# Optimization experiments

Measured on AMD Instinct MI355X. Metric: run time of the kernel, lower is better.

Reference implementation:

```python
import jax, jax.numpy as jnp
import numpy as np

B, S, L, CIN = 8, 32, 128, 1024
C1, C2 = 512, 256            # conv1_channel, conv2_channel
D1, D2 = 512, 128            # deconv1_channel, deconv2_channel
CD, SIM = 300, 128           # concept_dim, similarity_dim
L4 = L // 4


def _conv1d(x, w, b, pad):
    # x: [N, Cin, L], w: [Cout, Cin, k] (PyTorch layout)
    y = jax.lax.conv_general_dilated(x, w, (1,), [(pad, pad)],
                                     dimension_numbers=('NCH', 'OIH', 'NCH'))
    return y + b[None, :, None]


def _maxpool2(x):
    return jax.lax.reduce_window(x, -jnp.inf, jax.lax.max, (1, 1, 2), (1, 1, 2), 'VALID')


def _deconv1d(x, w, b):
    # PyTorch ConvTranspose1d(kernel=4, stride=2, padding=1); w: [Cin, Cout, k]
    w2 = jnp.flip(w, -1).transpose(1, 0, 2)  # -> OIH
    y = jax.lax.conv_general_dilated(x, w2, (1,), [(2, 2)], lhs_dilation=(2,),
                                     dimension_numbers=('NCH', 'OIH', 'NCH'))
    return y + b[None, :, None]


def setup_inputs():
    ks = jax.random.split(jax.random.key(0), 32)
    g = lambda i, shape: jax.random.normal(ks[i], shape, jnp.float32) * 0.02
    return {
        'batch': jax.random.normal(ks[0], (B, S, L, CIN), jnp.float32),
        'concept1': jax.random.normal(ks[1], (B, CD), jnp.float32),
        'concept2': jax.random.normal(ks[2], (B, CD), jnp.float32),
        'seg_len': jax.random.randint(ks[3], (B, S), 1, L + 1),
        'conv1_w': g(4, (C1, CIN, 5)), 'conv1_b': g(5, (C1,)),
        'conv2_w': g(6, (C2, C1, 5)), 'conv2_b': g(7, (C2,)),
        'sa_wq': g(8, (C2, C2)), 'sa_bq': g(9, (C2,)),
        'sa_wk': g(10, (C2, C2)), 'sa_bk': g(11, (C2,)),
        'sa_v': g(12, (C2,)), 'sa_vb': g(13, ()),
        'ca_wq': g(14, (CD, C2)), 'ca_bq': g(15, (C2,)),
        'ca_wk': g(16, (C2, C2)), 'ca_bk': g(17, (C2,)),
        'ca_v': g(18, (C2,)), 'ca_vb': g(19, ()),
        'dc1_w': g(20, (4 * C2, D1, 4)), 'dc1_b': g(21, (D1,)),
        'dc2_w': g(22, (D1, D2, 4)), 'dc2_b': g(23, (D2,)),
        'sim1_w': g(24, (D2, SIM)),
        'sim2_w': g(25, (CD, SIM)),
        'mlp_w': g(26, (SIM,)), 'mlp_b': g(27, ()),
    }


def reference(batch, concept1, concept2, seg_len,
              conv1_w, conv1_b, conv2_w, conv2_b,
              sa_wq, sa_bq, sa_wk, sa_bk, sa_v, sa_vb,
              ca_wq, ca_bq, ca_wk, ca_bk, ca_v, ca_vb,
              dc1_w, dc1_b, dc2_w, dc2_b,
              sim1_w, sim2_w, mlp_w, mlp_b):
    N = B * S
    # conv stack: [N, CIN, L] -> [N, C2, L/4]
    x = batch.reshape(N, L, CIN).transpose(0, 2, 1)
    t = _maxpool2(_conv1d(x, conv1_w, conv1_b, 2))
    t = _maxpool2(_conv1d(t, conv2_w, conv2_b, 2))
    tmp2 = t.transpose(0, 2, 1)                       # [N, L4, C2]

    # vectorized length mask: mask[i,j,k] = k < ceil(seg_len/4)  <=>  seg_len > 4k
    mask = (seg_len[:, :, None] > 4 * jnp.arange(L4)).reshape(N, 1, L4)

    # self additive attention over pooled positions
    qp = tmp2 @ sa_wq + sa_bq                          # [N, L4, H]
    kp = tmp2 @ sa_wk + sa_bk                          # [N, L4, H]
    s = jnp.einsum('nqkh,h->nqk', jnp.tanh(qp[:, :, None, :] + kp[:, None, :, :]), sa_v) + sa_vb
    s = jnp.where(mask, s, -1e9)
    a = jax.nn.softmax(s, axis=-1)                     # [N, L4, L4]
    self_res = jnp.einsum('nqk,nkc->nqc', a, tmp2)     # [N, L4, C2]

    # concept attention (query identical across positions -> compute once)
    ckp = tmp2 @ ca_wk + ca_bk                         # [N, L4, H]

    def concept_attn(c):
        cq = jnp.repeat(c @ ca_wq + ca_bq, S, axis=0)  # [N, H]
        sc = jnp.einsum('nkh,h->nk', jnp.tanh(cq[:, None, :] + ckp), ca_v) + ca_vb
        sc = jnp.where(mask[:, 0, :], sc, -1e9)
        ac = jax.nn.softmax(sc, axis=-1)               # [N, L4]
        r = jnp.einsum('nk,nkc->nc', ac, tmp2)         # [N, C2]
        return jnp.broadcast_to(r[:, None, :], (N, L4, C2))

    c1_res = concept_attn(concept1)
    c2_res = concept_attn(concept2)

    ar = jnp.concatenate([tmp2, self_res, c1_res, c2_res], axis=-1)  # [N, L4, 4*C2]
    r = _deconv1d(ar.transpose(0, 2, 1), dc1_w, dc1_b)               # [N, D1, L/2]
    r = _deconv1d(r, dc2_w, dc2_b).transpose(0, 2, 1)                # [N, L, D2]
    r = r.reshape(B, S * L, D2)

    sim1 = r @ sim1_w                                                # [B, S*L, SIM]

    def score(c):
        cs = (c @ sim2_w)[:, None, :] * sim1
        return jax.nn.sigmoid(cs @ mlp_w + mlp_b).reshape(B, S, L)

    return score(concept1), score(concept2)
```

## Files before the change

### kernel.cpp

```cpp
#include <hip/hip_runtime.h>
#include <cstdint>

typedef __bf16 bf16;
typedef __bf16 bf16x8 __attribute__((ext_vector_type(8)));
typedef float f32x4 __attribute__((ext_vector_type(4)));

__device__ __forceinline__ void gload_lds16(const void* g, void* l) {
  __builtin_amdgcn_global_load_lds(
      (const __attribute__((address_space(1))) unsigned int*)g,
      (__attribute__((address_space(3))) unsigned int*)l, 16, 0, 0);
}

__device__ __forceinline__ float tanh_fast(float x) {
  float ax = fabsf(x);
  float e = __expf(ax + ax);
  float t = 1.0f - 2.0f / (e + 1.0f);
  return x < 0.0f ? -t : t;
}

template<int MODE, int DEPTH>
__global__ __launch_bounds__(256) void gemm_tap(
    const bf16* __restrict__ A, const bf16* __restrict__ Bt,
    const float* __restrict__ bias, bf16* __restrict__ Out,
    const bf16* __restrict__ zp,
    int snA, int logP, int logCI, int shift0, int ntaps, int cbCount,
    int cbCI, int pairs, int Ktot, int COt, int snO,
    const float* __restrict__ uu, const float* __restrict__ mlpb,
    float* __restrict__ outF)
{
  __shared__ __align__(16) bf16 Ab[2 * DEPTH][4096];
  __shared__ __align__(16) bf16 Bb[2 * DEPTH][4096];
  const int tid  = threadIdx.x;
  const int wave = tid >> 6, lane = tid & 63;
  const int wr = wave >> 1, wc = wave & 1;
  const int m0  = blockIdx.x << 7;
  const int co0 = blockIdx.y << 7;
  const int P     = 1 << logP;
  const int Pmask = P - 1;
  const int CI    = 1 << logCI;
  f32x4 acc[4][4] = {};

  const int rowL = tid >> 2;
  const int kg   = tid & 3;
  const int fOff = ((kg ^ ((rowL + (rowL >> 2)) & 3)) << 3);

  const int mA0 = m0 + rowL,      nA0 = mA0 >> logP, pA0v = mA0 & Pmask;
  const int mA1 = m0 + rowL + 64, nA1 = mA1 >> logP, pA1v = mA1 & Pmask;
  const bf16* baseA0 = A + nA0 * snA + fOff;
  const bf16* baseA1 = A + nA1 * snA + fOff;
  const bf16* baseB0 = Bt + (co0 + rowL) * Ktot + fOff;
  const bf16* baseB1 = Bt + (co0 + rowL + 64) * Ktot + fOff;
  const bf16* zsrc = zp + fOff;

  const int frow  = lane & 15;
  const int rdOff = (((lane >> 4) ^ ((frow + (frow >> 2)) & 3)) << 3);

  for (int cb = 0; cb < cbCount; ++cb) {
    for (int tap = 0; tap < ntaps; ++tap) {
      const int sh = tap + shift0;
      const int rA0 = pA0v + sh, rA1 = pA1v + sh;
      const bool v0 = (unsigned)rA0 < (unsigned)P;
      const bool v1 = (unsigned)rA1 < (unsigned)P;
      const bf16* pa0 = v0 ? (baseA0 + rA0 * CI + cb * cbCI) : zsrc;
      const bf16* pa1 = v1 ? (baseA1 + rA1 * CI + cb * cbCI) : zsrc;
      const bf16* pb0 = baseB0 + (cb * ntaps + tap) * cbCI;
      const bf16* pb1 = baseB1 + (cb * ntaps + tap) * cbCI;

      for (int kc = 0; kc < pairs; kc += DEPTH) {
#pragma unroll
        for (int h = 0; h < 2 * DEPTH; ++h) {
          gload_lds16(pa0 + 32 * h, &Ab[h][wave * 512]);
          gload_lds16(pa1 + 32 * h, &Ab[h][2048 + wave * 512]);
          gload_lds16(pb0 + 32 * h, &Bb[h][wave * 512]);
          gload_lds16(pb1 + 32 * h, &Bb[h][2048 + wave * 512]);
        }
        if (v0) pa0 += 64 * DEPTH;
        if (v1) pa1 += 64 * DEPTH;
        pb0 += 64 * DEPTH; pb1 += 64 * DEPTH;
        __syncthreads();
#pragma unroll
        for (int h = 0; h < 2 * DEPTH; ++h) {
          bf16x8 af[4], bg[4];
#pragma unroll
          for (int i = 0; i < 4; ++i) {
            af[i] = *(const bf16x8*)&Ab[h][((wr << 6) + (i << 4) + frow) * 32 + rdOff];
            bg[i] = *(const bf16x8*)&Bb[h][((wc << 6) + (i << 4) + frow) * 32 + rdOff];
          }
#pragma unroll
          for (int i = 0; i < 4; ++i)
#pragma unroll
            for (int j = 0; j < 4; ++j)
              acc[i][j] = __builtin_amdgcn_mfma_f32_16x16x32_bf16(af[i], bg[j], acc[i][j], 0, 0, 0);
        }
        __syncthreads();
      }
    }
  }

  const int colL = lane & 15;
  const int rq   = (lane >> 4) << 2;

  if (MODE == 2) {
    float* scr0 = (float*)&Ab[0][0];
    float* scr1 = (float*)&Bb[0][0];
    const int n = m0 >> logP;
    const int b = n >> 5;
    const float* u0 = uu + b * 128;
    const float* u1 = uu + 1024 + b * 128;
#pragma unroll
    for (int i = 0; i < 4; ++i) {
#pragma unroll
      for (int r = 0; r < 4; ++r) {
        int rowLcl = (wr << 6) + (i << 4) + rq + r;
        float p0 = 0.0f, p1 = 0.0f;
#pragma unroll
        for (int j = 0; j < 4; ++j) {
          int gco = (wc << 6) + (j << 4) + colL;
          float v = acc[i][j][r];
          p0 += v * u0[gco];
          p1 += v * u1[gco];
        }
        scr0[rowLcl * 32 + (wc << 4) + colL] = p0;
        scr1[rowLcl * 32 + (wc << 4) + colL] = p1;
      }
    }
    __syncthreads();
    {
      int rowLcl = tid >> 1, c = tid & 1;
      const float* s = c ? scr1 : scr0;
      float sum = 0.0f;
#pragma unroll
      for (int k = 0; k < 32; ++k) sum += s[rowLcl * 32 + k];
      float val = 1.0f / (1.0f + __expf(-(sum + mlpb[0])));
      outF[(c ? 32768 : 0) + m0 + rowLcl] = val;
    }
    return;
  }

#pragma unroll
  for (int i = 0; i < 4; ++i) {
    int m = m0 + (wr << 6) + (i << 4) + rq;
    int n = m >> logP, p = m & Pmask;
#pragma unroll
    for (int j = 0; j < 4; ++j) {
      int gco = co0 + (wc << 6) + (j << 4) + colL;
      float bv = bias[gco];
      if (MODE == 1) {
        float v0 = fmaxf(acc[i][j][0], acc[i][j][1]) + bv;
        float v1 = fmaxf(acc[i][j][2], acc[i][j][3]) + bv;
        bf16* o = Out + n * snO + (p >> 1) * COt + gco;
        o[0]   = (bf16)v0;
        o[COt] = (bf16)v1;
      } else {
#pragma unroll
        for (int r = 0; r < 4; ++r)
          Out[n * snO + (p + r) * COt + gco] = (bf16)(acc[i][j][r] + bv);
      }
    }
  }
}

__global__ __launch_bounds__(256) void prep_all(
    const float* __restrict__ conv1_w, const float* __restrict__ conv2_w,
    const float* __restrict__ sa_wq, const float* __restrict__ sa_wk,
    const float* __restrict__ ca_wk, const float* __restrict__ dc1_w,
    const float* __restrict__ dc2_w, const float* __restrict__ sim1_w,
    const float* __restrict__ c1b, const float* __restrict__ c2b,
    const float* __restrict__ sabq, const float* __restrict__ sabk,
    const float* __restrict__ cabk, const float* __restrict__ d1b,
    const float* __restrict__ d2b,
    const float* __restrict__ c1, const float* __restrict__ c2,
    const float* __restrict__ ca_wq, const float* __restrict__ ca_bq,
    const float* __restrict__ sim2_w, const float* __restrict__ mlp_w,
    const float* __restrict__ batch, bf16* __restrict__ bb16,
    bf16* __restrict__ Bt1, bf16* __restrict__ Bt2, bf16* __restrict__ Bqkc,
    bf16* __restrict__ Btd1, bf16* __restrict__ Btd2, bf16* __restrict__ Bts1,
    float* __restrict__ bias, float* __restrict__ cq, float* __restrict__ uu)
{
  const int blk = blockIdx.x;
  if (blk >= 27492) {
    int idx = ((blk - 27492) * 256 + threadIdx.x) * 8;
    float4 a = *(const float4*)&batch[idx];
    float4 b = *(const float4*)&batch[idx + 4];
    bf16x8 v;
    v[0] = (bf16)a.x; v[1] = (bf16)a.y; v[2] = (bf16)a.z; v[3] = (bf16)a.w;
    v[4] = (bf16)b.x; v[5] = (bf16)b.y; v[6] = (bf16)b.z; v[7] = (bf16)b.w;
    *(bf16x8*)&bb16[idx] = v;
    return;
  }
  if (blk < 27468) {
    int idx = blk * 256 + threadIdx.x;
    if (idx < 3072) {
      if (idx < 2944) {
        float v;
        if (idx < 512)       v = c1b[idx];
        else if (idx < 768)  v = c2b[idx - 512];
        else if (idx < 1024) v = sabq[idx - 768];
        else if (idx < 1280) v = sabk[idx - 1024];
        else if (idx < 1536) v = cabk[idx - 1280];
        else if (idx < 2560) v = d1b[(idx - 1536) & 511];
        else if (idx < 2816) v = d2b[(idx - 2560) & 127];
        else                 v = 0.0f;
        bias[idx] = v;
      }
    } else if (idx < 2624512) {
      int i = idx - 3072;
      int co = i / 5120, r = i - co * 5120;
      int cb = r / 1280, r2 = r - cb * 1280;
      int tap = r2 >> 8, cl = r2 & 255;
      Bt1[i] = (bf16)conv1_w[co * 5120 + (cb * 256 + cl) * 5 + tap];
    } else if (idx < 3279872) {
      int i = idx - 2624512;
      int co = i / 2560, r = i - co * 2560;
      int cb = r / 1280, r2 = r - cb * 1280;
      int tap = r2 >> 8, cl = r2 & 255;
      Bt2[i] = (bf16)conv2_w[co * 2560 + (cb * 256 + cl) * 5 + tap];
    } else if (idx < 3476480) {
      int i = idx - 3279872;
      int co = i >> 8, ci = i & 255;
      float v;
      if (co < 256)      v = sa_wq[ci * 256 + co];
      else if (co < 512) v = sa_wk[ci * 256 + (co - 256)];
      else               v = ca_wk[ci * 256 + (co - 512)];
      Bqkc[i] = (bf16)v;
    } else if (idx < 6622208) {
      int i = idx - 3476480;
      int co = i / 3072, r = i - co * 3072;
      int cb = r / 768, r2 = r - cb * 768;
      int tap = r2 >> 8, cl = r2 & 255;
      int ci = cb * 256 + cl;
      int par = co >> 9, c = co & 511;
      int ki = -1;
      if (par == 0) { if (tap == 1) ki = 1; else if (tap == 0) ki = 3; }
      else          { if (tap == 2) ki = 0; else if (tap == 1) ki = 2; }
      Btd1[i] = (ki >= 0) ? (bf16)dc1_w[ci * 2048 + c * 4 + ki] : (bf16)0.0f;
    } else if (idx < 7015424) {
      int i = idx - 6622208;
      int co = i / 1536, r = i - co * 1536;
      int cb = r / 768, r2 = r - cb * 768;
      int tap = r2 >> 8, cl = r2 & 255;
      int ci = cb * 256 + cl;
      int par = co >> 7, c = co & 127;
      int ki = -1;
      if (par == 0) { if (tap == 1) ki = 1; else if (tap == 0) ki = 3; }
      else          { if (tap == 2) ki = 0; else if (tap == 1) ki = 2; }
      Btd2[i] = (ki >= 0) ? (bf16)dc2_w[ci * 512 + c * 4 + ki] : (bf16)0.0f;
    } else {
      int i = idx - 7015424;
      int co = i >> 7, ci = i & 127;
      Bts1[i] = (bf16)sim1_w[ci * 128 + co];
    }
  } else {
    int sub = blk - 27468;
    if (sub < 16) {
      int o = sub * 256 + threadIdx.x;
      int c = o >> 11, b = (o >> 8) & 7, h = o & 255;
      const float* cc = (c ? c2 : c1) + b * 300;
      float acc = ca_bq[h];
      for (int j = 0; j < 300; ++j)
        acc += cc[j] * ca_wq[j * 256 + h];
      cq[o] = acc;
    } else {
      int o = (sub - 16) * 256 + threadIdx.x;
      int c = o >> 10, b = (o >> 7) & 7, m = o & 127;
      const float* cc = (c ? c2 : c1) + b * 300;
      float acc = 0.0f;
      for (int j = 0; j < 300; ++j)
        acc += cc[j] * sim2_w[j * 128 + m];
      uu[o] = acc * mlp_w[m];
    }
  }
}

__global__ __launch_bounds__(256) void kattn(
    const bf16* __restrict__ tmp2, const bf16* __restrict__ qkc,
    const float* __restrict__ sa_v, const float* __restrict__ sa_vb,
    const float* __restrict__ ca_v, const float* __restrict__ ca_vb,
    const float* __restrict__ cq, const int* __restrict__ seg,
    bf16* __restrict__ ar)
{
  const int n = blockIdx.x, tid = threadIdx.x;
  __shared__ __align__(16) bf16 t2[32 * 264];
  __shared__ __align__(16) bf16 bufA[32 * 264];
  __shared__ __align__(16) bf16 bufB[32 * 264];
  __shared__ float sv_s[256], cv_s[256];
  __shared__ float sbc[66];
  __shared__ float sbs[32 * 33];
  const int sl = seg[n];

#pragma unroll
  for (int rr = 0; rr < 4; ++rr) {
    int q = tid + (rr << 8);
    int k = q >> 5, c8 = (q & 31) << 3;
    *(uint4*)&t2[k * 264 + c8]   = *(const uint4*)&tmp2[n * 8192 + k * 256 + c8];
    *(uint4*)&bufA[k * 264 + c8] = *(const uint4*)&qkc[n * 24576 + k * 768 + 512 + c8];
  }
  sv_s[tid] = sa_v[tid];
  cv_s[tid] = ca_v[tid];
  __syncthreads();

  if (tid < 64) {
    int c = tid >> 5, k = tid & 31;
    const float* cqr = cq + (c * 8 + (n >> 5)) * 256;
    float acc = 0.0f;
    for (int h = 0; h < 256; ++h)
      acc += tanh_fast(cqr[h] + (float)bufA[k * 264 + h]) * cv_s[h];
    float sc = acc + ca_vb[0];
    sbc[c * 33 + k] = (sl > (k << 2)) ? sc : -1e9f;
  }
  __syncthreads();

#pragma unroll
  for (int rr = 0; rr < 4; ++rr) {
    int q = tid + (rr << 8);
    int k = q >> 5, c8 = (q & 31) << 3;
    *(uint4*)&bufB[k * 264 + c8] = *(const uint4*)&qkc[n * 24576 + k * 768 + c8];
    *(uint4*)&bufA[k * 264 + c8] = *(const uint4*)&qkc[n * 24576 + k * 768 + 256 + c8];
  }
  if (tid < 2) {
    float* row = &sbc[tid * 33];
    float mx = -1e30f;
    for (int k = 0; k < 32; ++k) mx = fmaxf(mx, row[k]);
    float sum = 0.0f;
    for (int k = 0; k < 32; ++k) { float e = __expf(row[k] - mx); row[k] = e; sum += e; }
    float inv = 1.0f / sum;
    for (int k = 0; k < 32; ++k) row[k] *= inv;
  }
  __syncthreads();

  {
    int col = tid;
    float rr0 = 0.0f, rr1 = 0.0f;
    for (int k = 0; k < 32; ++k) {
      float tv = (float)t2[k * 264 + col];
      rr0 += sbc[k] * tv;
      rr1 += sbc[33 + k] * tv;
    }
    bf16 b0 = (bf16)rr0, b1 = (bf16)rr1;
    bf16* arn = ar + n * 32768;
    for (int q = 0; q < 32; ++q) {
      arn[q * 1024 + col]       = t2[q * 264 + col];
      arn[q * 1024 + 512 + col] = b0;
      arn[q * 1024 + 768 + col] = b1;
    }
  }
  {
    float svb = sa_vb[0];
#pragma unroll
    for (int rr = 0; rr < 4; ++rr) {
      int id = tid + (rr << 8);
      int q = id >> 5, k = id & 31;
      float acc = 0.0f;
      for (int h = 0; h < 256; ++h)
        acc += tanh_fast((float)bufB[q * 264 + h] + (float)bufA[k * 264 + h]) * sv_s[h];
      float sc = acc + svb;
      sbs[q * 33 + k] = (sl > (k << 2)) ? sc : -1e9f;
    }
  }
  __syncthreads();

  if (tid < 32) {
    float* row = &sbs[tid * 33];
    float mx = -1e30f;
    for (int k = 0; k < 32; ++k) mx = fmaxf(mx, row[k]);
    float sum = 0.0f;
    for (int k = 0; k < 32; ++k) { float e = __expf(row[k] - mx); row[k] = e; sum += e; }
    float inv = 1.0f / sum;
    for (int k = 0; k < 32; ++k) row[k] *= inv;
  }
  __syncthreads();

  {
    int col = tid;
    bf16* arn = ar + n * 32768;
    for (int q = 0; q < 32; ++q) {
      float acc = 0.0f;
      for (int k = 0; k < 32; ++k)
        acc += sbs[q * 33 + k] * (float)t2[k * 264 + col];
      arn[q * 1024 + 256 + col] = (bf16)acc;
    }
  }
}

extern "C" void kernel_launch(void* const* d_in, const int* in_sizes, int n_in,
                              void* d_out, int out_size, void* d_ws, size_t ws_size,
                              hipStream_t stream) {
  const float* batch    = (const float*)d_in[0];
  const float* concept1 = (const float*)d_in[1];
  const float* concept2 = (const float*)d_in[2];
  const int*   seg      = (const int*)d_in[3];
  const float* conv1_w  = (const float*)d_in[4];
  const float* conv1_b  = (const float*)d_in[5];
  const float* conv2_w  = (const float*)d_in[6];
  const float* conv2_b  = (const float*)d_in[7];
  const float* sa_wq    = (const float*)d_in[8];
  const float* sa_bq    = (const float*)d_in[9];
  const float* sa_wk    = (const float*)d_in[10];
  const float* sa_bk    = (const float*)d_in[11];
  const float* sa_v     = (const float*)d_in[12];
  const float* sa_vb    = (const float*)d_in[13];
  const float* ca_wq    = (const float*)d_in[14];
  const float* ca_bq    = (const float*)d_in[15];
  const float* ca_wk    = (const float*)d_in[16];
  const float* ca_bk    = (const float*)d_in[17];
  const float* ca_v     = (const float*)d_in[18];
  const float* ca_vb    = (const float*)d_in[19];
  const float* dc1_w    = (const float*)d_in[20];
  const float* dc1_b    = (const float*)d_in[21];
  const float* dc2_w    = (const float*)d_in[22];
  const float* dc2_b    = (const float*)d_in[23];
  const float* sim1_w   = (const float*)d_in[24];
  const float* sim2_w   = (const float*)d_in[25];
  const float* mlp_w    = (const float*)d_in[26];
  const float* mlp_b    = (const float*)d_in[27];

  char* ws = (char*)d_ws;
  bf16* bb16  = (bf16*)(ws + 0);
  bf16* qkcb  = (bf16*)(ws + 0);
  bf16* arb   = (bf16*)(ws + 12582912);
  bf16* d1    = (bf16*)(ws + 29360128);
  bf16* rbuf  = (bf16*)(ws + 46137344);
  bf16* t1    = (bf16*)(ws + 67108864);
  bf16* tmp2b = (bf16*)(ws + 83886080);
  bf16* Bt1   = (bf16*)(ws + 88080384);
  bf16* Bt2   = (bf16*)(ws + 93323264);
  bf16* Bqkc  = (bf16*)(ws + 94633984);
  bf16* Btd1  = (bf16*)(ws + 95027200);
  bf16* Btd2  = (bf16*)(ws + 101318656);
  bf16* Bts1  = (bf16*)(ws + 102105088);
  float* biasall = (float*)(ws + 102137856);
  float* cqb  = (float*)(ws + 102149632);
  float* uub  = (float*)(ws + 102166016);
  const bf16* zp = (const bf16*)(biasall + 2816);
  float* outp = (float*)d_out;

  prep_all<<<43876, 256, 0, stream>>>(
      conv1_w, conv2_w, sa_wq, sa_wk, ca_wk, dc1_w, dc2_w, sim1_w,
      conv1_b, conv2_b, sa_bq, sa_bk, ca_bk, dc1_b, dc2_b,
      concept1, concept2, ca_wq, ca_bq, sim2_w, mlp_w,
      batch, bb16,
      Bt1, Bt2, Bqkc, Btd1, Btd2, Bts1, biasall, cqb, uub);

  gemm_tap<1, 1><<<dim3(256, 4), 256, 0, stream>>>(
      bb16, Bt1, biasall + 0, t1, zp, 131072, 7, 10, -2, 5, 4, 256, 4, 5120, 512, 32768,
      nullptr, nullptr, nullptr);

  gemm_tap<1, 2><<<dim3(128, 2), 256, 0, stream>>>(
      t1, Bt2, biasall + 512, tmp2b, zp, 32768, 6, 9, -2, 5, 2, 256, 4, 2560, 256, 8192,
      nullptr, nullptr, nullptr);

  gemm_tap<0, 2><<<dim3(64, 6), 256, 0, stream>>>(
      tmp2b, Bqkc, biasall + 768, qkcb, zp, 8192, 5, 8, 0, 1, 1, 256, 4, 256, 768, 24576,
      nullptr, nullptr, nullptr);

  kattn<<<256, 256, 0, stream>>>(tmp2b, qkcb, sa_v, sa_vb, ca_v, ca_vb, cqb, seg, arb);

  gemm_tap<0, 2><<<dim3(64, 8), 256, 0, stream>>>(
      arb, Btd1, biasall + 1536, d1, zp, 32768, 5, 10, -1, 3, 4, 256, 4, 3072, 1024, 32768,
      nullptr, nullptr, nullptr);

  gemm_tap<0, 2><<<dim3(128, 2), 256, 0, stream>>>(
      d1, Btd2, biasall + 2560, rbuf, zp, 32768, 6, 9, -1, 3, 2, 256, 4, 1536, 256, 16384,
      nullptr, nullptr, nullptr);

  gemm_tap<2, 2><<<dim3(256, 1), 256, 0, stream>>>(
      rbuf, Bts1, biasall + 2816, nullptr, zp, 16384, 7, 7, 0, 1, 1, 128, 2, 128, 128, 16384,
      uub, mlp_b, outp);
}
```

Baseline: 709.4 us.

## Use 256x256-tile 8-wave pipelined GEMM for conv1 with fused maxpool

```diff
diff --git a/kernel.cpp b/kernel.cpp
--- a/kernel.cpp
+++ b/kernel.cpp
@@ -156,6 +156,118 @@
         for (int r = 0; r < 4; ++r)
           Out[n * snO + (p + r) * COt + gco] = (bf16)(acc[i][j][r] + bv);
       }
+    }
+  }
+}
+
+template<int MH, int KS>
+__device__ __forceinline__ void phase8(
+    const bf16 (&Ab)[2][2][8192], const bf16 (&Bb)[2][2][8192],
+    f32x4 (&acc)[8][4], int buf, int wr, int wc, int frow, int rdOff)
+{
+  bf16x8 af[4], bg[4];
+#pragma unroll
+  for (int ii = 0; ii < 4; ++ii)
+    af[ii] = *(const bf16x8*)&Ab[buf][KS][((wr << 7) + (MH << 6) + (ii << 4) + frow) * 32 + rdOff];
+#pragma unroll
+  for (int j = 0; j < 4; ++j)
+    bg[j] = *(const bf16x8*)&Bb[buf][KS][((wc << 6) + (j << 4) + frow) * 32 + rdOff];
+  __builtin_amdgcn_s_barrier();
+  __builtin_amdgcn_s_setprio(1);
+#pragma unroll
+  for (int ii = 0; ii < 4; ++ii)
+#pragma unroll
+    for (int j = 0; j < 4; ++j)
+      acc[(MH << 2) + ii][j] =
+          __builtin_amdgcn_mfma_f32_16x16x32_bf16(af[ii], bg[j], acc[(MH << 2) + ii][j], 0, 0, 0);
+  __builtin_amdgcn_s_setprio(0);
+}
+
+template<int LOGP, int LOGCI, int SH0, int NTAPS, int CBCNT, int CBCI>
+__global__ __launch_bounds__(512, 2) void gemm8_pool(
+    const bf16* __restrict__ A, const bf16* __restrict__ Bt,
+    const float* __restrict__ bias, bf16* __restrict__ Out,
+    const bf16* __restrict__ zp, int snA, int Ktot, int COt, int snO)
+{
+  __shared__ __align__(16) bf16 Ab[2][2][8192];
+  __shared__ __align__(16) bf16 Bb[2][2][8192];
+  constexpr int P = 1 << LOGP, CI = 1 << LOGCI;
+  constexpr int KPC = CBCI / 64;
+  constexpr int NT = CBCNT * NTAPS * KPC;
+
+  const int tid = threadIdx.x;
+  const int wave = tid >> 6, lane = tid & 63;
+  const int wr = wave >> 2, wc = wave & 3;
+  const int m0 = blockIdx.x << 8, co0 = blockIdx.y << 8;
+  const int n0 = m0 >> LOGP;
+
+  f32x4 acc[8][4] = {};
+
+  const int rowP = tid >> 2;
+  const int kOff = (((tid & 3) ^ ((rowP + (rowP >> 2)) & 3)) << 3);
+  const bf16* baseA = A + n0 * snA + kOff;
+  const bf16* baseB = Bt + (co0 + rowP) * Ktot + kOff;
+  const bf16* zsrc = zp + kOff;
+  const int ldsW = wave << 9;
+
+  const int frow = lane & 15;
+  const int rdOff = (((lane >> 4) ^ ((frow + (frow >> 2)) & 3)) << 3);
+
+  auto stageA = [&](int u, int kh, int bfs) {
+    int cb = u / (NTAPS * KPC);
+    int rem = u - cb * (NTAPS * KPC);
+    int tap = rem / KPC;
+    int kc = rem - tap * KPC;
+    int rA = rowP + tap + SH0;
+    bool v = (unsigned)rA < (unsigned)P;
+    const bf16* p0 = v ? baseA + rA * CI + cb * CBCI + kc * 64 + kh * 32 : zsrc;
+    const bf16* p1 = v ? p0 + snA : zsrc;
+    gload_lds16(p0, &Ab[bfs][kh][ldsW]);
+    gload_lds16(p1, &Ab[bfs][kh][ldsW + 4096]);
+  };
+  auto stageB = [&](int u, int kh, int bfs) {
+    const bf16* p0 = baseB + u * 64 + kh * 32;
+    gload_lds16(p0, &Bb[bfs][kh][ldsW]);
+    gload_lds16(p0 + 128 * Ktot, &Bb[bfs][kh][ldsW + 4096]);
+  };
+
+  stageA(0, 0, 0); stageB(0, 0, 0);
+  stageA(0, 1, 0); stageB(0, 1, 0);
+  stageA(1, 0, 1); stageB(1, 0, 1);
+  asm volatile("s_waitcnt vmcnt(4)" ::: "memory");
+  __builtin_amdgcn_s_barrier();
+
+#pragma unroll 1
+  for (int t = 0; t < NT; ++t) {
+    const int buf = t & 1;
+    if (t + 1 < NT) stageA(t + 1, 1, buf ^ 1);
+    phase8<0, 0>(Ab, Bb, acc, buf, wr, wc, frow, rdOff);
+    __builtin_amdgcn_s_barrier();
+    if (t + 1 < NT) stageB(t + 1, 1, buf ^ 1);
+    phase8<1, 0>(Ab, Bb, acc, buf, wr, wc, frow, rdOff);
+    __builtin_amdgcn_s_barrier();
+    if (t + 2 < NT) stageA(t + 2, 0, buf);
+    phase8<0, 1>(Ab, Bb, acc, buf, wr, wc, frow, rdOff);
+    __builtin_amdgcn_s_barrier();
+    if (t + 2 < NT) stageB(t + 2, 0, buf);
+    phase8<1, 1>(Ab, Bb, acc, buf, wr, wc, frow, rdOff);
+    if (t < NT - 2) { asm volatile("s_waitcnt vmcnt(4)" ::: "memory"); }
+    else            { asm volatile("s_waitcnt vmcnt(0)" ::: "memory"); }
+    __builtin_amdgcn_s_barrier();
+  }
+
+  const int colL = lane & 15, rq = (lane >> 4) << 2;
+#pragma unroll
+  for (int i = 0; i < 8; ++i) {
+    int m = m0 + (wr << 7) + (i << 4) + rq;
+    int n = m >> LOGP, p = m & (P - 1);
+    bf16* orow = Out + n * snO + (p >> 1) * COt;
+#pragma unroll
+    for (int j = 0; j < 4; ++j) {
+      int gco = co0 + (wc << 6) + (j << 4) + colL;
+      float bv = bias[gco];
+      orow[gco]       = (bf16)(fmaxf(acc[i][j][0], acc[i][j][1]) + bv);
+      orow[COt + gco] = (bf16)(fmaxf(acc[i][j][2], acc[i][j][3]) + bv);
     }
   }
 }
@@ -441,9 +553,8 @@
       batch, bb16,
       Bt1, Bt2, Bqkc, Btd1, Btd2, Bts1, biasall, cqb, uub);
 
-  gemm_tap<1, 1><<<dim3(256, 4), 256, 0, stream>>>(
-      bb16, Bt1, biasall + 0, t1, zp, 131072, 7, 10, -2, 5, 4, 256, 4, 5120, 512, 32768,
-      nullptr, nullptr, nullptr);
+  gemm8_pool<7, 10, -2, 5, 4, 256><<<dim3(128, 2), 512, 0, stream>>>(
+      bb16, Bt1, biasall + 0, t1, zp, 131072, 5120, 512, 32768);
 
   gemm_tap<1, 2><<<dim3(128, 2), 256, 0, stream>>>(
       t1, Bt2, biasall + 512, tmp2b, zp, 32768, 6, 9, -2, 5, 2, 256, 4, 2560, 256, 8192,
```

After: 701.0 us. Within noise of the previous version (-1.2%).

## Double-buffer GEMM K-tiles with flattened loop and overlapped LDS prefetch

Applied to the files above, without the earlier changes.

```diff
diff --git a/kernel.cpp b/kernel.cpp
--- a/kernel.cpp
+++ b/kernel.cpp
@@ -4,11 +4,18 @@
 typedef __bf16 bf16;
 typedef __bf16 bf16x8 __attribute__((ext_vector_type(8)));
 typedef float f32x4 __attribute__((ext_vector_type(4)));
+typedef __attribute__((address_space(3))) bf16 lds_bf16;
 
 __device__ __forceinline__ void gload_lds16(const void* g, void* l) {
   __builtin_amdgcn_global_load_lds(
       (const __attribute__((address_space(1))) unsigned int*)g,
       (__attribute__((address_space(3))) unsigned int*)l, 16, 0, 0);
+}
+
+__device__ __forceinline__ bf16x8 ld_b128(const lds_bf16* p) {
+  bf16x8 r;
+  asm volatile("ds_read_b128 %0, %1" : "=v"(r) : "v"(p));
+  return r;
 }
 
 __device__ __forceinline__ float tanh_fast(float x) {
@@ -18,8 +25,8 @@
   return x < 0.0f ? -t : t;
 }
 
-template<int MODE, int DEPTH>
-__global__ __launch_bounds__(256) void gemm_tap(
+template<int MODE>
+__global__ __launch_bounds__(256, 2) void gemm_tap(
     const bf16* __restrict__ A, const bf16* __restrict__ Bt,
     const float* __restrict__ bias, bf16* __restrict__ Out,
     const bf16* __restrict__ zp,
@@ -28,8 +35,9 @@
     const float* __restrict__ uu, const float* __restrict__ mlpb,
     float* __restrict__ outF)
 {
-  __shared__ __align__(16) bf16 Ab[2 * DEPTH][4096];
-  __shared__ __align__(16) bf16 Bb[2 * DEPTH][4096];
+  __shared__ __align__(16) bf16 Ab[2][2][4096];
+  __shared__ __align__(16) bf16 Bb[2][2][4096];
+  (void)pairs;
   const int tid  = threadIdx.x;
   const int wave = tid >> 6, lane = tid & 63;
   const int wr = wave >> 1, wc = wave & 1;
@@ -55,54 +63,79 @@
   const int frow  = lane & 15;
   const int rdOff = (((lane >> 4) ^ ((frow + (frow >> 2)) & 3)) << 3);
 
-  for (int cb = 0; cb < cbCount; ++cb) {
-    for (int tap = 0; tap < ntaps; ++tap) {
-      const int sh = tap + shift0;
-      const int rA0 = pA0v + sh, rA1 = pA1v + sh;
-      const bool v0 = (unsigned)rA0 < (unsigned)P;
-      const bool v1 = (unsigned)rA1 < (unsigned)P;
-      const bf16* pa0 = v0 ? (baseA0 + rA0 * CI + cb * cbCI) : zsrc;
-      const bf16* pa1 = v1 ? (baseA1 + rA1 * CI + cb * cbCI) : zsrc;
-      const bf16* pb0 = baseB0 + (cb * ntaps + tap) * cbCI;
-      const bf16* pb1 = baseB1 + (cb * ntaps + tap) * cbCI;
-
-      for (int kc = 0; kc < pairs; kc += DEPTH) {
-#pragma unroll
-        for (int h = 0; h < 2 * DEPTH; ++h) {
-          gload_lds16(pa0 + 32 * h, &Ab[h][wave * 512]);
-          gload_lds16(pa1 + 32 * h, &Ab[h][2048 + wave * 512]);
-          gload_lds16(pb0 + 32 * h, &Bb[h][wave * 512]);
-          gload_lds16(pb1 + 32 * h, &Bb[h][2048 + wave * 512]);
-        }
-        if (v0) pa0 += 64 * DEPTH;
-        if (v1) pa1 += 64 * DEPTH;
-        pb0 += 64 * DEPTH; pb1 += 64 * DEPTH;
-        __syncthreads();
-#pragma unroll
-        for (int h = 0; h < 2 * DEPTH; ++h) {
-          bf16x8 af[4], bg[4];
-#pragma unroll
-          for (int i = 0; i < 4; ++i) {
-            af[i] = *(const bf16x8*)&Ab[h][((wr << 6) + (i << 4) + frow) * 32 + rdOff];
-            bg[i] = *(const bf16x8*)&Bb[h][((wc << 6) + (i << 4) + frow) * 32 + rdOff];
-          }
-#pragma unroll
-          for (int i = 0; i < 4; ++i)
-#pragma unroll
-            for (int j = 0; j < 4; ++j)
-              acc[i][j] = __builtin_amdgcn_mfma_f32_16x16x32_bf16(af[i], bg[j], acc[i][j], 0, 0, 0);
-        }
-        __syncthreads();
-      }
-    }
+  const int ksA = wave & 1, ksB = ksA ^ 1;
+
+  const int kpc = cbCI >> 6;
+  const int NT  = cbCount * ntaps * kpc;
+  int s_kc = 0, s_tap = 0, s_cb = 0;
+
+  auto stageTile = [&](int bfs) {
+    int sh  = s_tap + shift0;
+    int rA0 = pA0v + sh, rA1 = pA1v + sh;
+    int ko  = s_cb * cbCI + (s_kc << 6);
+    const bf16* pa0 = ((unsigned)rA0 < (unsigned)P) ? baseA0 + rA0 * CI + ko : zsrc;
+    const bf16* pa1 = ((unsigned)rA1 < (unsigned)P) ? baseA1 + rA1 * CI + ko : zsrc;
+    const bf16* pb0 = baseB0 + (s_cb * ntaps + s_tap) * cbCI + (s_kc << 6);
+    const bf16* pb1 = baseB1 + (s_cb * ntaps + s_tap) * cbCI + (s_kc << 6);
+    gload_lds16(pa0,      &Ab[bfs][0][wave * 512]);
+    gload_lds16(pa0 + 32, &Ab[bfs][1][wave * 512]);
+    gload_lds16(pa1,      &Ab[bfs][0][2048 + wave * 512]);
+    gload_lds16(pa1 + 32, &Ab[bfs][1][2048 + wave * 512]);
+    gload_lds16(pb0,      &Bb[bfs][0][wave * 512]);
+    gload_lds16(pb0 + 32, &Bb[bfs][1][wave * 512]);
+    gload_lds16(pb1,      &Bb[bfs][0][2048 + wave * 512]);
+    gload_lds16(pb1 + 32, &Bb[bfs][1][2048 + wave * 512]);
+    if (++s_kc == kpc) { s_kc = 0; if (++s_tap == ntaps) { s_tap = 0; ++s_cb; } }
+  };
+
+  stageTile(0);
+  __syncthreads();
+
+  bf16x8 a0[4], a1[4], b0f[4], b1f[4];
+
+#pragma unroll 1
+  for (int t = 0; t < NT; ++t) {
+    const int buf = t & 1;
+#pragma unroll
+    for (int i = 0; i < 4; ++i)
+      a0[i] = ld_b128((const lds_bf16*)&Ab[buf][ksA][((wr << 6) + (i << 4) + frow) * 32 + rdOff]);
+#pragma unroll
+    for (int j = 0; j < 4; ++j)
+      b0f[j] = ld_b128((const lds_bf16*)&Bb[buf][ksA][((wc << 6) + (j << 4) + frow) * 32 + rdOff]);
+    if (t + 1 < NT) stageTile(buf ^ 1);
+#pragma unroll
+    for (int i = 0; i < 4; ++i)
+      a1[i] = ld_b128((const lds_bf16*)&Ab[buf][ksB][((wr << 6) + (i << 4) + frow) * 32 + rdOff]);
+#pragma unroll
+    for (int j = 0; j < 4; ++j)
+      b1f[j] = ld_b128((const lds_bf16*)&Bb[buf][ksB][((wc << 6) + (j << 4) + frow) * 32 + rdOff]);
+    asm volatile("s_waitcnt lgkmcnt(8)" ::: "memory");
+    __builtin_amdgcn_sched_barrier(0);
+    __builtin_amdgcn_s_setprio(1);
+#pragma unroll
+    for (int i = 0; i < 4; ++i)
+#pragma unroll
+      for (int j = 0; j < 4; ++j)
+        acc[i][j] = __builtin_amdgcn_mfma_f32_16x16x32_bf16(a0[i], b0f[j], acc[i][j], 0, 0, 0);
+    __builtin_amdgcn_s_setprio(0);
+    asm volatile("s_waitcnt lgkmcnt(0)" ::: "memory");
+    __builtin_amdgcn_sched_barrier(0);
+    __builtin_amdgcn_s_setprio(1);
+#pragma unroll
+    for (int i = 0; i < 4; ++i)
+#pragma unroll
+      for (int j = 0; j < 4; ++j)
+        acc[i][j] = __builtin_amdgcn_mfma_f32_16x16x32_bf16(a1[i], b1f[j], acc[i][j], 0, 0, 0);
+    __builtin_amdgcn_s_setprio(0);
+    __syncthreads();
   }
 
   const int colL = lane & 15;
   const int rq   = (lane >> 4) << 2;
 
   if (MODE == 2) {
-    float* scr0 = (float*)&Ab[0][0];
-    float* scr1 = (float*)&Bb[0][0];
+    float* scr0 = (float*)&Ab[0][0][0];
+    float* scr1 = (float*)&Bb[0][0][0];
     const int n = m0 >> logP;
     const int b = n >> 5;
     const float* u0 = uu + b * 128;
@@ -441,29 +474,29 @@
       batch, bb16,
       Bt1, Bt2, Bqkc, Btd1, Btd2, Bts1, biasall, cqb, uub);
 
-  gemm_tap<1, 1><<<dim3(256, 4), 256, 0, stream>>>(
+  gemm_tap<1><<<dim3(256, 4), 256, 0, stream>>>(
       bb16, Bt1, biasall + 0, t1, zp, 131072, 7, 10, -2, 5, 4, 256, 4, 5120, 512, 32768,
       nullptr, nullptr, nullptr);
 
-  gemm_tap<1, 2><<<dim3(128, 2), 256, 0, stream>>>(
+  gemm_tap<1><<<dim3(128, 2), 256, 0, stream>>>(
       t1, Bt2, biasall + 512, tmp2b, zp, 32768, 6, 9, -2, 5, 2, 256, 4, 2560, 256, 8192,
       nullptr, nullptr, nullptr);
 
-  gemm_tap<0, 2><<<dim3(64, 6), 256, 0, stream>>>(
+  gemm_tap<0><<<dim3(64, 6), 256, 0, stream>>>(
       tmp2b, Bqkc, biasall + 768, qkcb, zp, 8192, 5, 8, 0, 1, 1, 256, 4, 256, 768, 24576,
       nullptr, nullptr, nullptr);
 
   kattn<<<256, 256, 0, stream>>>(tmp2b, qkcb, sa_v, sa_vb, ca_v, ca_vb, cqb, seg, arb);
 
-  gemm_tap<0, 2><<<dim3(64, 8), 256, 0, stream>>>(
+  gemm_tap<0><<<dim3(64, 8), 256, 0, stream>>>(
       arb, Btd1, biasall + 1536, d1, zp, 32768, 5, 10, -1, 3, 4, 256, 4, 3072, 1024, 32768,
       nullptr, nullptr, nullptr);
 
-  gemm_tap<0, 2><<<dim3(128, 2), 256, 0, stream>>>(
+  gemm_tap<0><<<dim3(128, 2), 256, 0, stream>>>(
       d1, Btd2, biasall + 2560, rbuf, zp, 32768, 6, 9, -1, 3, 2, 256, 4, 1536, 256, 16384,
       nullptr, nullptr, nullptr);
 
-  gemm_tap<2, 2><<<dim3(256, 1), 256, 0, stream>>>(
+  gemm_tap<2><<<dim3(256, 1), 256, 0, stream>>>(
       rbuf, Bts1, biasall + 2816, nullptr, zp, 16384, 7, 7, 0, 1, 1, 128, 2, 128, 128, 16384,
       uub, mlp_b, outp);
 }
```

Result: faster. 652.7 us (-8.0%).
